# Performance work log

Measured on AMD Instinct MI355X. Metric: run time of the kernel, lower is better.

Reference implementation:

```python
import jax, jax.numpy as jnp
import numpy as np

D_K = 64
SCALE = jnp.sqrt(jnp.float32(D_K))

def setup_inputs() -> dict:
    key = jax.random.key(0)
    kq, kk, kv = jax.random.split(key, 3)
    shape = (2, 16, 2048, D_K)  # [batch, heads, seq, d_k]
    return {
        "Q": jax.random.normal(kq, shape, dtype=jnp.float32),
        "K": jax.random.normal(kk, shape, dtype=jnp.float32),
        "V": jax.random.normal(kv, shape, dtype=jnp.float32),
    }

def reference(Q, K, V):
    # scores: [B, H, S, S]
    scores = jnp.einsum("bhqd,bhkd->bhqk", Q, K) / SCALE
    weights = jax.nn.softmax(scores, axis=-1)
    return jnp.einsum("bhqk,bhkd->bhqd", weights, V)
```

## Files before the change

### kernel.cpp

```cpp
#include <hip/hip_runtime.h>
#include <math.h>

#define S_LEN 2048
#define DK 64
#define BH 32
#define NT 32
#define TILE_US 8192
#define TILE_B  16384

#if defined(__has_builtin)
#if __has_builtin(__builtin_amdgcn_exp2f)
#define EXP2F(x) __builtin_amdgcn_exp2f(x)
#else
#define EXP2F(x) exp2f(x)
#endif
#else
#define EXP2F(x) exp2f(x)
#endif

typedef _Float16 f16x8 __attribute__((ext_vector_type(8)));
typedef __fp16   fp16x2 __attribute__((ext_vector_type(2)));
typedef float    f32x16 __attribute__((ext_vector_type(16)));

#define MFMAH(a,b,c) __builtin_amdgcn_mfma_f32_32x32x16_f16((a),(b),(c),0,0,0)

union U16H { uint4 u; f16x8 h; unsigned short s[8]; };

__device__ __forceinline__ f16x8 g16(const unsigned short* p){
    U16H t; t.u = *(const uint4*)p; return t.h;
}
__device__ __forceinline__ f16x8 u4h(unsigned a, unsigned b, unsigned c, unsigned d){
    U16H t; t.u = make_uint4(a,b,c,d); return t.h;
}
__device__ __forceinline__ unsigned pk16(float a, float b){
    union { fp16x2 h; unsigned u; } c;
    c.h = __builtin_amdgcn_cvt_pkrtz(a, b);
    return c.u;
}

__global__ __launch_bounds__(256) void prep(const float* __restrict__ K,
                                            const float* __restrict__ V,
                                            unsigned short* __restrict__ W) {
    __shared__ __align__(16) float Vs[64 * 68];
    const int t = threadIdx.x;
    const int head = blockIdx.x >> 5;
    const int kb = blockIdx.x & 31;
    const size_t hbase = (size_t)head * S_LEN * DK;
    unsigned short* Wt = W + (size_t)(head * NT + kb) * TILE_US;

    {
        const int row = t >> 2;
        const int c0 = (t & 3) * 16;
        const float* vp = V + hbase + (size_t)(kb * 64 + row) * DK + c0;
        #pragma unroll
        for (int i = 0; i < 4; ++i)
            *(float4*)(Vs + row * 68 + c0 + 4 * i) = *(const float4*)(vp + 4 * i);
    }
    #pragma unroll
    for (int i = 0; i < 2; ++i) {
        const int P = i * 256 + t;
        const int frag = P >> 6, lane8 = P & 63;
        const int pos = ((frag >> 2) << 5) | (lane8 & 31);
        const int q  = pos & 15;
        const int kl = (((q >> 2) & 1) << 3) | (q & 3) | (((q >> 3) & 1) << 2);
        const int r  = (pos & 48) | kl;
        const int p  = ((frag & 3) << 1) | (lane8 >> 5);
        const float* kp = K + hbase + (size_t)(kb * 64 + r) * DK + p * 8;
        const float4 a = *(const float4*)kp;
        const float4 b = *(const float4*)(kp + 4);
        *(uint4*)(Wt + P * 8) = make_uint4(pk16(a.x, a.y), pk16(a.z, a.w),
                                           pk16(b.x, b.y), pk16(b.z, b.w));
    }
    __syncthreads();
    #pragma unroll
    for (int i = 0; i < 2; ++i) {
        const int P = i * 256 + t;
        const int frag = P >> 6, lane8 = P & 63;
        const int d  = ((frag >> 2) << 5) | (lane8 & 31);
        const int k0 = (frag & 3) * 16 + (lane8 >> 5) * 8;
        const float* c = Vs + k0 * 68 + d;
        const float v0 = c[0],   v1 = c[68],  v2 = c[136], v3 = c[204];
        const float v4 = c[272], v5 = c[340], v6 = c[408], v7 = c[476];
        *(uint4*)(Wt + 4096 + P * 8) =
            make_uint4(pk16(v0, v1), pk16(v2, v3), pk16(v4, v5), pk16(v6, v7));
    }
}

#define PHASE(SC0, SC1, SN0, SN1, KNa, KNb, KPa, KPb, tKp, tVp)                 \
  {                                                                             \
    float ra0 = 0.f, ra1 = 0.f;                                                 \
    _Pragma("unroll")                                                           \
    for (int r = 0; r < 16; ++r) {                                              \
      SC0[r] = EXP2F(SC0[r]); ra0 += SC0[r];                                    \
      SC1[r] = EXP2F(SC1[r]); ra1 += SC1[r];                                    \
    }                                                                           \
    lsum += ra0 + ra1;                                                          \
    unsigned P2[2][4][2];                                                       \
    _Pragma("unroll")                                                           \
    for (int b = 0; b < 4; ++b) {                                               \
      P2[0][b][0] = pk16(SC0[4*b+0], SC0[4*b+1]);                               \
      P2[0][b][1] = pk16(SC0[4*b+2], SC0[4*b+3]);                               \
      P2[1][b][0] = pk16(SC1[4*b+0], SC1[4*b+1]);                               \
      P2[1][b][1] = pk16(SC1[4*b+2], SC1[4*b+3]);                               \
    }                                                                           \
    SN0 = zzero; SN1 = zzero;                                                   \
    __builtin_amdgcn_s_setprio(1);                                              \
    _Pragma("unroll")                                                           \
    for (int ks = 0; ks < 4; ++ks) {                                            \
      SN0 = MFMAH(KNa[ks], qf[ks], SN0);                                        \
      SN1 = MFMAH(KNb[ks], qf[ks], SN1);                                        \
    }                                                                           \
    __builtin_amdgcn_s_setprio(0);                                              \
    _Pragma("unroll")                                                           \
    for (int ks = 0; ks < 4; ++ks) {                                            \
      KPa[ks] = g16((tKp) + ks * 512 + lo);                                     \
      KPb[ks] = g16((tKp) + (4 + ks) * 512 + lo);                               \
    }                                                                           \
    _Pragma("unroll")                                                           \
    for (int ks = 0; ks < 4; ++ks) {                                            \
      const int mt = ks >> 1, kk2 = (ks & 1) * 2;                               \
      const f16x8 ph = u4h(P2[mt][kk2][0],   P2[mt][kk2][1],                    \
                           P2[mt][kk2+1][0], P2[mt][kk2+1][1]);                 \
      __builtin_amdgcn_s_setprio(1);                                            \
      o0 = MFMAH(va[ks], ph, o0);                                               \
      o1 = MFMAH(vb[ks], ph, o1);                                               \
      __builtin_amdgcn_s_setprio(0);                                            \
    }                                                                           \
    _Pragma("unroll")                                                           \
    for (int ks = 0; ks < 4; ++ks) {                                            \
      va[ks] = g16((tVp) + (8 + ks) * 512 + lo);                                \
      vb[ks] = g16((tVp) + (12 + ks) * 512 + lo);                               \
    }                                                                           \
  }

__global__ __launch_bounds__(256, 2) void fa4(const float* __restrict__ Q,
                                              const unsigned short* __restrict__ W,
                                              float* __restrict__ O) {
    const int tid  = threadIdx.x;
    const int w    = tid >> 6;
    const int lane = tid & 63;
    const int L31  = tid & 31;
    const int q5   = (tid >> 5) & 1;

    const int bid  = blockIdx.x;
    const int x    = bid & 7, g = bid >> 3;
    const int head = ((g >> 4) << 3) | x;
    const int qb   = g & 15;
    const size_t hbase = (size_t)head * S_LEN * DK;
    const unsigned short* Wh = W + (size_t)head * NT * TILE_US;

    const float c1 = 0.18033688011112042f;
    f16x8 qf[4];
    {
        const int qrow = qb * 128 + w * 32 + L31;
        const float* qp = Q + hbase + (size_t)qrow * DK;
        #pragma unroll
        for (int ks = 0; ks < 4; ++ks) {
            const float4 a = *(const float4*)(qp + ks * 16 + q5 * 8);
            const float4 b = *(const float4*)(qp + ks * 16 + q5 * 8 + 4);
            qf[ks] = u4h(pk16(a.x * c1, a.y * c1), pk16(a.z * c1, a.w * c1),
                         pk16(b.x * c1, b.y * c1), pk16(b.z * c1, b.w * c1));
        }
    }

    const int lo = lane * 8;
    const f32x16 zzero = {};
    f16x8 kAa[4], kAb[4], kBa[4], kBb[4], va[4], vb[4];

    #pragma unroll
    for (int ks = 0; ks < 4; ++ks) {
        kAa[ks] = g16(Wh + ks * 512 + lo);
        kAb[ks] = g16(Wh + (4 + ks) * 512 + lo);
    }
    f32x16 sE0 = zzero, sE1 = zzero;
    __builtin_amdgcn_s_setprio(1);
    #pragma unroll
    for (int ks = 0; ks < 4; ++ks) {
        sE0 = MFMAH(kAa[ks], qf[ks], sE0);
        sE1 = MFMAH(kAb[ks], qf[ks], sE1);
    }
    __builtin_amdgcn_s_setprio(0);
    #pragma unroll
    for (int ks = 0; ks < 4; ++ks) {
        kBa[ks] = g16(Wh + TILE_US + ks * 512 + lo);
        kBb[ks] = g16(Wh + TILE_US + (4 + ks) * 512 + lo);
    }
    #pragma unroll
    for (int ks = 0; ks < 4; ++ks) {
        va[ks] = g16(Wh + (8 + ks) * 512 + lo);
        vb[ks] = g16(Wh + (12 + ks) * 512 + lo);
    }

    f32x16 o0 = zzero, o1 = zzero;
    f32x16 sO0, sO1;
    float lsum = 0.f;

    for (int t = 0; t < NT; t += 2) {
        const unsigned short* tn1 = Wh + (size_t)(t + 1) * TILE_US;
        const unsigned short* tn2 = Wh + (size_t)(t + 2) * TILE_US;
        const unsigned short* tn3 = Wh + (size_t)(t + 3) * TILE_US;
        PHASE(sE0, sE1, sO0, sO1, kBa, kBb, kAa, kAb, tn2, tn1)
        PHASE(sO0, sO1, sE0, sE1, kAa, kAb, kBa, kBb, tn3, tn2)
    }

    const float inv = 1.f / (lsum + __shfl_xor(lsum, 32));
    const int qrow = qb * 128 + w * 32 + L31;
    float* op = O + hbase + (size_t)qrow * DK;
    #pragma unroll
    for (int b = 0; b < 4; ++b) {
        float4 o;
        o.x = o0[4*b+0] * inv; o.y = o0[4*b+1] * inv;
        o.z = o0[4*b+2] * inv; o.w = o0[4*b+3] * inv;
        *(float4*)(op + 8 * b + 4 * q5) = o;
        o.x = o1[4*b+0] * inv; o.y = o1[4*b+1] * inv;
        o.z = o1[4*b+2] * inv; o.w = o1[4*b+3] * inv;
        *(float4*)(op + 32 + 8 * b + 4 * q5) = o;
    }
}

extern "C" void kernel_launch(void* const* d_in, const int* in_sizes, int n_in,
                              void* d_out, int out_size, void* d_ws, size_t ws_size,
                              hipStream_t stream) {
    const float* Q = (const float*)d_in[0];
    const float* K = (const float*)d_in[1];
    const float* V = (const float*)d_in[2];
    float* O = (float*)d_out;
    unsigned short* W = (unsigned short*)d_ws;
    prep<<<dim3(BH * NT), dim3(256), 0, stream>>>(K, V, W);
    fa4<<<dim3(512), dim3(256), 0, stream>>>(Q, W, O);
}
```

Measured before the change: 135.5 us.

## Fuse K/V fp16 conversion into attention kernel via double-buffered LDS

Removes the separate prep kernel that converted K and V to fp16 fragment layout in a workspace. The attention kernel now loads fp32 K/V tiles from global memory, packs them to fp16 into double-buffered shared memory, and reads MFMA fragments from LDS, with __syncthreads per tile. This avoids one kernel launch and the workspace round trip. In exchange, each of the 16 query blocks per head redoes the conversion, V is read with strided scalar loads, and the previous two-phase software-pipelined register prefetch is replaced by simpler LDS staging with barriers.

```diff
diff --git a/kernel.cpp b/kernel.cpp
--- a/kernel.cpp
+++ b/kernel.cpp
@@ -5,8 +5,6 @@
 #define DK 64
 #define BH 32
 #define NT 32
-#define TILE_US 8192
-#define TILE_B  16384
 
 #if defined(__has_builtin)
 #if __has_builtin(__builtin_amdgcn_exp2f)
@@ -26,7 +24,7 @@
 
 union U16H { uint4 u; f16x8 h; unsigned short s[8]; };
 
-__device__ __forceinline__ f16x8 g16(const unsigned short* p){
+__device__ __forceinline__ f16x8 ldsh8(const unsigned short* p){
     U16H t; t.u = *(const uint4*)p; return t.h;
 }
 __device__ __forceinline__ f16x8 u4h(unsigned a, unsigned b, unsigned c, unsigned d){
@@ -38,104 +36,43 @@
     return c.u;
 }
 
-__global__ __launch_bounds__(256) void prep(const float* __restrict__ K,
-                                            const float* __restrict__ V,
-                                            unsigned short* __restrict__ W) {
-    __shared__ __align__(16) float Vs[64 * 68];
-    const int t = threadIdx.x;
-    const int head = blockIdx.x >> 5;
-    const int kb = blockIdx.x & 31;
-    const size_t hbase = (size_t)head * S_LEN * DK;
-    unsigned short* Wt = W + (size_t)(head * NT + kb) * TILE_US;
-
-    {
-        const int row = t >> 2;
-        const int c0 = (t & 3) * 16;
-        const float* vp = V + hbase + (size_t)(kb * 64 + row) * DK + c0;
-        #pragma unroll
-        for (int i = 0; i < 4; ++i)
-            *(float4*)(Vs + row * 68 + c0 + 4 * i) = *(const float4*)(vp + 4 * i);
-    }
-    #pragma unroll
-    for (int i = 0; i < 2; ++i) {
-        const int P = i * 256 + t;
-        const int frag = P >> 6, lane8 = P & 63;
-        const int pos = ((frag >> 2) << 5) | (lane8 & 31);
-        const int q  = pos & 15;
-        const int kl = (((q >> 2) & 1) << 3) | (q & 3) | (((q >> 3) & 1) << 2);
-        const int r  = (pos & 48) | kl;
-        const int p  = ((frag & 3) << 1) | (lane8 >> 5);
-        const float* kp = K + hbase + (size_t)(kb * 64 + r) * DK + p * 8;
-        const float4 a = *(const float4*)kp;
-        const float4 b = *(const float4*)(kp + 4);
-        *(uint4*)(Wt + P * 8) = make_uint4(pk16(a.x, a.y), pk16(a.z, a.w),
-                                           pk16(b.x, b.y), pk16(b.z, b.w));
-    }
-    __syncthreads();
-    #pragma unroll
-    for (int i = 0; i < 2; ++i) {
-        const int P = i * 256 + t;
-        const int frag = P >> 6, lane8 = P & 63;
-        const int d  = ((frag >> 2) << 5) | (lane8 & 31);
-        const int k0 = (frag & 3) * 16 + (lane8 >> 5) * 8;
-        const float* c = Vs + k0 * 68 + d;
-        const float v0 = c[0],   v1 = c[68],  v2 = c[136], v3 = c[204];
-        const float v4 = c[272], v5 = c[340], v6 = c[408], v7 = c[476];
-        *(uint4*)(Wt + 4096 + P * 8) =
-            make_uint4(pk16(v0, v1), pk16(v2, v3), pk16(v4, v5), pk16(v6, v7));
-    }
-}
-
-#define PHASE(SC0, SC1, SN0, SN1, KNa, KNb, KPa, KPb, tKp, tVp)                 \
+#define LOADT(tl)                                                               \
   {                                                                             \
-    float ra0 = 0.f, ra1 = 0.f;                                                 \
+    const float* kp0_ = K + hbase + (size_t)((tl) * 64 + kR0) * DK + kP0 * 8;   \
+    k0a = *(const float4*)kp0_;  k0b = *(const float4*)(kp0_ + 4);              \
+    const float* kp1_ = K + hbase + (size_t)((tl) * 64 + kR1) * DK + kP1 * 8;   \
+    k1a = *(const float4*)kp1_;  k1b = *(const float4*)(kp1_ + 4);              \
+    const float* vp0_ = V + hbase + (size_t)((tl) * 64 + vK0) * DK + vD0;       \
     _Pragma("unroll")                                                           \
-    for (int r = 0; r < 16; ++r) {                                              \
-      SC0[r] = EXP2F(SC0[r]); ra0 += SC0[r];                                    \
-      SC1[r] = EXP2F(SC1[r]); ra1 += SC1[r];                                    \
-    }                                                                           \
-    lsum += ra0 + ra1;                                                          \
-    unsigned P2[2][4][2];                                                       \
+    for (int j = 0; j < 8; ++j) vr0[j] = vp0_[j * DK];                          \
+    const float* vp1_ = V + hbase + (size_t)((tl) * 64 + vK1) * DK + vD1;       \
     _Pragma("unroll")                                                           \
-    for (int b = 0; b < 4; ++b) {                                               \
-      P2[0][b][0] = pk16(SC0[4*b+0], SC0[4*b+1]);                               \
-      P2[0][b][1] = pk16(SC0[4*b+2], SC0[4*b+3]);                               \
-      P2[1][b][0] = pk16(SC1[4*b+0], SC1[4*b+1]);                               \
-      P2[1][b][1] = pk16(SC1[4*b+2], SC1[4*b+3]);                               \
-    }                                                                           \
-    SN0 = zzero; SN1 = zzero;                                                   \
-    __builtin_amdgcn_s_setprio(1);                                              \
-    _Pragma("unroll")                                                           \
-    for (int ks = 0; ks < 4; ++ks) {                                            \
-      SN0 = MFMAH(KNa[ks], qf[ks], SN0);                                        \
-      SN1 = MFMAH(KNb[ks], qf[ks], SN1);                                        \
-    }                                                                           \
-    __builtin_amdgcn_s_setprio(0);                                              \
-    _Pragma("unroll")                                                           \
-    for (int ks = 0; ks < 4; ++ks) {                                            \
-      KPa[ks] = g16((tKp) + ks * 512 + lo);                                     \
-      KPb[ks] = g16((tKp) + (4 + ks) * 512 + lo);                               \
-    }                                                                           \
-    _Pragma("unroll")                                                           \
-    for (int ks = 0; ks < 4; ++ks) {                                            \
-      const int mt = ks >> 1, kk2 = (ks & 1) * 2;                               \
-      const f16x8 ph = u4h(P2[mt][kk2][0],   P2[mt][kk2][1],                    \
-                           P2[mt][kk2+1][0], P2[mt][kk2+1][1]);                 \
-      __builtin_amdgcn_s_setprio(1);                                            \
-      o0 = MFMAH(va[ks], ph, o0);                                               \
-      o1 = MFMAH(vb[ks], ph, o1);                                               \
-      __builtin_amdgcn_s_setprio(0);                                            \
-    }                                                                           \
-    _Pragma("unroll")                                                           \
-    for (int ks = 0; ks < 4; ++ks) {                                            \
-      va[ks] = g16((tVp) + (8 + ks) * 512 + lo);                                \
-      vb[ks] = g16((tVp) + (12 + ks) * 512 + lo);                               \
-    }                                                                           \
+    for (int j = 0; j < 8; ++j) vr1[j] = vp1_[j * DK];                          \
   }
 
-__global__ __launch_bounds__(256, 2) void fa4(const float* __restrict__ Q,
-                                              const unsigned short* __restrict__ W,
+#define WRITET(b)                                                               \
+  {                                                                             \
+    *(uint4*)&KB[b][tid * 8] =                                                  \
+        make_uint4(pk16(k0a.x, k0a.y), pk16(k0a.z, k0a.w),                      \
+                   pk16(k0b.x, k0b.y), pk16(k0b.z, k0b.w));                     \
+    *(uint4*)&KB[b][(tid + 256) * 8] =                                          \
+        make_uint4(pk16(k1a.x, k1a.y), pk16(k1a.z, k1a.w),                      \
+                   pk16(k1b.x, k1b.y), pk16(k1b.z, k1b.w));                     \
+    *(uint4*)&VB[b][tid * 8] =                                                  \
+        make_uint4(pk16(vr0[0], vr0[1]), pk16(vr0[2], vr0[3]),                  \
+                   pk16(vr0[4], vr0[5]), pk16(vr0[6], vr0[7]));                 \
+    *(uint4*)&VB[b][(tid + 256) * 8] =                                          \
+        make_uint4(pk16(vr1[0], vr1[1]), pk16(vr1[2], vr1[3]),                  \
+                   pk16(vr1[4], vr1[5]), pk16(vr1[6], vr1[7]));                 \
+  }
+
+__global__ __launch_bounds__(256, 2) void fa5(const float* __restrict__ Q,
+                                              const float* __restrict__ K,
+                                              const float* __restrict__ V,
                                               float* __restrict__ O) {
+    __shared__ __align__(16) unsigned short KB[2][4096];
+    __shared__ __align__(16) unsigned short VB[2][4096];
+
     const int tid  = threadIdx.x;
     const int w    = tid >> 6;
     const int lane = tid & 63;
@@ -147,7 +84,30 @@
     const int head = ((g >> 4) << 3) | x;
     const int qb   = g & 15;
     const size_t hbase = (size_t)head * S_LEN * DK;
-    const unsigned short* Wh = W + (size_t)head * NT * TILE_US;
+
+    int kR0, kP0, kR1, kP1, vD0, vK0, vD1, vK1;
+    {
+        const int P0 = tid,  f0 = P0 >> 6, l80 = P0 & 63;
+        const int P1 = tid + 256, f1 = P1 >> 6, l81 = P1 & 63;
+        {
+            const int pos = ((f0 >> 2) << 5) | (l80 & 31);
+            const int q = pos & 15;
+            const int kl = (((q >> 2) & 1) << 3) | (q & 3) | (((q >> 3) & 1) << 2);
+            kR0 = (pos & 48) | kl;
+            kP0 = ((f0 & 3) << 1) | (l80 >> 5);
+        }
+        {
+            const int pos = ((f1 >> 2) << 5) | (l81 & 31);
+            const int q = pos & 15;
+            const int kl = (((q >> 2) & 1) << 3) | (q & 3) | (((q >> 3) & 1) << 2);
+            kR1 = (pos & 48) | kl;
+            kP1 = ((f1 & 3) << 1) | (l81 >> 5);
+        }
+        vD0 = ((f0 >> 2) << 5) | (l80 & 31);
+        vK0 = (f0 & 3) * 16 + (l80 >> 5) * 8;
+        vD1 = ((f1 >> 2) << 5) | (l81 & 31);
+        vK1 = (f1 & 3) * 16 + (l81 >> 5) * 8;
+    }
 
     const float c1 = 0.18033688011112042f;
     f16x8 qf[4];
@@ -163,44 +123,64 @@
         }
     }
 
-    const int lo = lane * 8;
+    float4 k0a, k0b, k1a, k1b;
+    float  vr0[8], vr1[8];
     const f32x16 zzero = {};
-    f16x8 kAa[4], kAb[4], kBa[4], kBb[4], va[4], vb[4];
-
-    #pragma unroll
-    for (int ks = 0; ks < 4; ++ks) {
-        kAa[ks] = g16(Wh + ks * 512 + lo);
-        kAb[ks] = g16(Wh + (4 + ks) * 512 + lo);
-    }
-    f32x16 sE0 = zzero, sE1 = zzero;
-    __builtin_amdgcn_s_setprio(1);
-    #pragma unroll
-    for (int ks = 0; ks < 4; ++ks) {
-        sE0 = MFMAH(kAa[ks], qf[ks], sE0);
-        sE1 = MFMAH(kAb[ks], qf[ks], sE1);
-    }
-    __builtin_amdgcn_s_setprio(0);
-    #pragma unroll
-    for (int ks = 0; ks < 4; ++ks) {
-        kBa[ks] = g16(Wh + TILE_US + ks * 512 + lo);
-        kBb[ks] = g16(Wh + TILE_US + (4 + ks) * 512 + lo);
-    }
-    #pragma unroll
-    for (int ks = 0; ks < 4; ++ks) {
-        va[ks] = g16(Wh + (8 + ks) * 512 + lo);
-        vb[ks] = g16(Wh + (12 + ks) * 512 + lo);
-    }
-
     f32x16 o0 = zzero, o1 = zzero;
-    f32x16 sO0, sO1;
     float lsum = 0.f;
 
-    for (int t = 0; t < NT; t += 2) {
-        const unsigned short* tn1 = Wh + (size_t)(t + 1) * TILE_US;
-        const unsigned short* tn2 = Wh + (size_t)(t + 2) * TILE_US;
-        const unsigned short* tn3 = Wh + (size_t)(t + 3) * TILE_US;
-        PHASE(sE0, sE1, sO0, sO1, kBa, kBb, kAa, kAb, tn2, tn1)
-        PHASE(sO0, sO1, sE0, sE1, kAa, kAb, kBa, kBb, tn3, tn2)
+    LOADT(0)
+    WRITET(0)
+    __syncthreads();
+    LOADT(1)
+
+    for (int t = 0; t < NT; ++t) {
+        const int cur = t & 1;
+        if (t + 1 < NT) { WRITET(cur ^ 1) }
+        __syncthreads();
+        if (t + 2 < NT) { LOADT(t + 2) }
+
+        f32x16 s0 = zzero, s1 = zzero;
+        __builtin_amdgcn_s_setprio(1);
+        #pragma unroll
+        for (int ks = 0; ks < 4; ++ks) {
+            const f16x8 ka = ldsh8(&KB[cur][ks * 512 + lane * 8]);
+            const f16x8 kb = ldsh8(&KB[cur][(4 + ks) * 512 + lane * 8]);
+            s0 = MFMAH(ka, qf[ks], s0);
+            s1 = MFMAH(kb, qf[ks], s1);
+        }
+        __builtin_amdgcn_s_setprio(0);
+
+        float ra0 = 0.f, ra1 = 0.f;
+        #pragma unroll
+        for (int r = 0; r < 16; ++r) {
+            s0[r] = EXP2F(s0[r]); ra0 += s0[r];
+            s1[r] = EXP2F(s1[r]); ra1 += s1[r];
+        }
+        lsum += ra0 + ra1;
+
+        unsigned P2[2][4][2];
+        #pragma unroll
+        for (int b = 0; b < 4; ++b) {
+            P2[0][b][0] = pk16(s0[4*b+0], s0[4*b+1]);
+            P2[0][b][1] = pk16(s0[4*b+2], s0[4*b+3]);
+            P2[1][b][0] = pk16(s1[4*b+0], s1[4*b+1]);
+            P2[1][b][1] = pk16(s1[4*b+2], s1[4*b+3]);
+        }
+
+        #pragma unroll
+        for (int ks = 0; ks < 4; ++ks) {
+            const int mt = ks >> 1, kk2 = (ks & 1) * 2;
+            const f16x8 va = ldsh8(&VB[cur][ks * 512 + lane * 8]);
+            const f16x8 vb = ldsh8(&VB[cur][(4 + ks) * 512 + lane * 8]);
+            const f16x8 ph = u4h(P2[mt][kk2][0],   P2[mt][kk2][1],
+                                 P2[mt][kk2+1][0], P2[mt][kk2+1][1]);
+            __builtin_amdgcn_s_setprio(1);
+            o0 = MFMAH(va, ph, o0);
+            o1 = MFMAH(vb, ph, o1);
+            __builtin_amdgcn_s_setprio(0);
+        }
+        __syncthreads();
     }
 
     const float inv = 1.f / (lsum + __shfl_xor(lsum, 32));
@@ -225,7 +205,6 @@
     const float* K = (const float*)d_in[1];
     const float* V = (const float*)d_in[2];
     float* O = (float*)d_out;
-    unsigned short* W = (unsigned short*)d_ws;
-    prep<<<dim3(BH * NT), dim3(256), 0, stream>>>(K, V, W);
-    fa4<<<dim3(512), dim3(256), 0, stream>>>(Q, W, O);
-}
+    (void)d_ws; (void)ws_size;
+    fa5<<<dim3(512), dim3(256), 0, stream>>>(Q, K, V, O);
+}
```

After: 132.3 us (median of 2 runs). -2.4%, faster.
